# Performance work log

Measured on AMD Instinct MI355X. Metric: run time of the kernel, lower is better.

The kernel has to match this reference:

```python
import jax, jax.numpy as jnp
import numpy as np

N, E, DIN, DH, DOUT = 100000, 1600000, 512, 128, 40


def setup_inputs() -> dict:
    key = jax.random.key(0)
    ks = jax.random.split(key, 4)
    x = jax.random.normal(ks[0], (N, DIN), dtype=jnp.float32)
    edge_index = jax.random.randint(ks[1], (2, E), 0, N, dtype=jnp.int32)
    W1 = jax.random.normal(ks[2], (DIN, DH), dtype=jnp.float32) / np.sqrt(DIN).astype(np.float32)
    b1 = jnp.zeros((DH,), jnp.float32)
    W2 = jax.random.normal(ks[3], (DH, DOUT), dtype=jnp.float32) / np.sqrt(DH).astype(np.float32)
    b2 = jnp.zeros((DOUT,), jnp.float32)
    return {"x": x, "edge_index": edge_index, "W1": W1, "b1": b1, "W2": W2, "b2": b2}


def _gcn_conv(x, W, b, src, dst, norm, n):
    # PyG GCNConv: linear transform first, then normalized neighbor aggregation
    h = x @ W                                   # [n, d_out]
    msg = h[src] * norm[:, None]                # gather + scale, [E+n, d_out]
    out = jax.ops.segment_sum(msg, dst, num_segments=n)  # scatter-add
    return out + b


def reference(x, edge_index, W1, b1, W2, b2):
    n = x.shape[0]
    loops = jnp.arange(n, dtype=edge_index.dtype)
    src = jnp.concatenate([edge_index[0], loops])   # with self-loops
    dst = jnp.concatenate([edge_index[1], loops])
    deg = jax.ops.segment_sum(jnp.ones_like(dst, dtype=jnp.float32), dst, num_segments=n)
    dinv = jnp.where(deg > 0, jax.lax.rsqrt(jnp.maximum(deg, 1.0)), 0.0)
    norm = dinv[src] * dinv[dst]                    # deg^{-1/2}[j] * deg^{-1/2}[i]
    h = jax.nn.relu(_gcn_conv(x, W1, b1, src, dst, norm, n))
    # dropout p=0.5 is a no-op in eval mode (training=False)
    h = _gcn_conv(h, W2, b2, src, dst, norm, n)
    return h, jax.nn.log_softmax(h, axis=1)
```

## Files before the change

### kernel.cpp

```cpp
#include <hip/hip_runtime.h>
#include <math.h>


typedef unsigned int uint;
typedef unsigned short ushort_t;
using short8  = __attribute__((ext_vector_type(8))) short;
using float4v = __attribute__((ext_vector_type(4))) float;

__device__ __forceinline__ ushort_t f2bf(float f) {
    uint u = __float_as_uint(f);
    u += 0x7FFFu + ((u >> 16) & 1u);
    return (ushort_t)(u >> 16);
}
__device__ __forceinline__ float2 unpack2(uint v) {
    return make_float2(__uint_as_float(v << 16), __uint_as_float(v & 0xFFFF0000u));
}
__device__ __forceinline__ uint pack2(float a, float b) {
    return (uint)f2bf(a) | ((uint)f2bf(b) << 16);
}


__global__ __launch_bounds__(256) void k_bhist(const int* __restrict__ dst,
                                               int* __restrict__ bcnt, int e, int nb) {
    __shared__ int h[800];
    for (int t = threadIdx.x; t < nb; t += 256) h[t] = 0;
    __syncthreads();
    int ibase = blockIdx.x * 2560 + threadIdx.x;
#pragma unroll
    for (int j = 0; j < 10; j++) {
        int i = ibase + j * 256;
        if (i < e) atomicAdd(&h[dst[i] >> 7], 1);
    }
    __syncthreads();
    for (int t = threadIdx.x; t < nb; t += 256) {
        int c = h[t];
        if (c) atomicAdd(&bcnt[t], c);
    }
}

__global__ __launch_bounds__(256) void k_bscan(const int* __restrict__ bcnt, int* __restrict__ bbase,
                                               int* __restrict__ bcur, int* __restrict__ row_ptr,
                                               int nb, int n, int e) {
    __shared__ int sd[256];
    int t = threadIdx.x;
    int base = t * 4;
    int v[4];
#pragma unroll
    for (int j = 0; j < 4; j++) v[j] = (base + j < nb) ? bcnt[base + j] : 0;
    int s0 = v[0], s1 = s0 + v[1], s2 = s1 + v[2], s3 = s2 + v[3];
    sd[t] = s3;
    __syncthreads();
    for (int d = 1; d < 256; d <<= 1) {
        int x = (t >= d) ? sd[t - d] : 0;
        __syncthreads();
        sd[t] += x;
        __syncthreads();
    }
    int excl = sd[t] - s3;
    int pre0 = excl, pre1 = excl + s0, pre2 = excl + s1, pre3 = excl + s2;
    if (base + 0 < nb) { bbase[base + 0] = pre0; bcur[base + 0] = pre0; }
    if (base + 1 < nb) { bbase[base + 1] = pre1; bcur[base + 1] = pre1; }
    if (base + 2 < nb) { bbase[base + 2] = pre2; bcur[base + 2] = pre2; }
    if (base + 3 < nb) { bbase[base + 3] = pre3; bcur[base + 3] = pre3; }
    if (t == 255) bbase[nb] = excl + s3;
    if (t == 0) row_ptr[n] = e;
}

__global__ __launch_bounds__(256) void k_part(const int* __restrict__ src, const int* __restrict__ dst,
                                              int* __restrict__ bcur, uint* __restrict__ pbuf,
                                              int e, int nb) {
    __shared__ int h[800];
    __shared__ int base_l[800];
    for (int t = threadIdx.x; t < nb; t += 256) h[t] = 0;
    __syncthreads();
    uint pk[10]; int bk[10]; int lp[10];
    int ibase = blockIdx.x * 2560 + threadIdx.x;
#pragma unroll
    for (int j = 0; j < 10; j++) {
        int i = ibase + j * 256;
        bk[j] = -1;
        if (i < e) {
            int s = src[i], d = dst[i];
            int b = d >> 7;
            bk[j] = b;
            pk[j] = ((uint)(d & 127) << 25) | (uint)s;
            lp[j] = atomicAdd(&h[b], 1);
        }
    }
    __syncthreads();
    for (int t = threadIdx.x; t < nb; t += 256) {
        int c = h[t];
        base_l[t] = c ? atomicAdd(&bcur[t], c) : 0;
    }
    __syncthreads();
#pragma unroll
    for (int j = 0; j < 10; j++) {
        if (bk[j] >= 0) pbuf[base_l[bk[j]] + lp[j]] = pk[j];
    }
}

__global__ __launch_bounds__(256) void k_bsort(const uint* __restrict__ pbuf,
                                               const int* __restrict__ bbase,
                                               float* __restrict__ dinv,
                                               int* __restrict__ row_ptr,
                                               int* __restrict__ es_src, int n) {
    __shared__ int cl[128];
    __shared__ int cur[128];
    const int b = blockIdx.x;
    const int tid = threadIdx.x;
    const int ebeg = bbase[b], eend = bbase[b + 1];
    const int m = eend - ebeg;
    if (tid < 128) cl[tid] = 0;
    __syncthreads();
    for (int i = tid; i < m; i += 256) {
        uint p = pbuf[ebeg + i];
        atomicAdd(&cl[p >> 25], 1);
    }
    __syncthreads();
    int own = (tid < 128) ? cl[tid] : 0;
    for (int d = 1; d < 128; d <<= 1) {
        int v = 0;
        if (tid < 128 && tid >= d) v = cl[tid - d];
        __syncthreads();
        if (tid < 128 && tid >= d) cl[tid] += v;
        __syncthreads();
    }
    if (tid < 128) {
        int excl = cl[tid] - own;
        int node = b * 128 + tid;
        if (node < n) {
            dinv[node] = rsqrtf((float)(own + 1));
            row_ptr[node] = ebeg + excl;
        }
        cur[tid] = excl;
    }
    __syncthreads();
    for (int i = tid; i < m; i += 256) {
        uint p = pbuf[ebeg + i];
        int dl = (int)(p >> 25);
        int pos = atomicAdd(&cur[dl], 1);
        es_src[ebeg + pos] = (int)(p & 0x1FFFFFFu);
    }
}

__global__ __launch_bounds__(256) void k_wprep(const float* __restrict__ W1,
                                               const float* __restrict__ W2,
                                               ushort_t* __restrict__ W1t,
                                               ushort_t* __restrict__ W2t) {
    int idx = blockIdx.x * 256 + threadIdx.x;
    if (idx < 65536) {
        int nn = idx >> 9, k = idx & 511;
        W1t[idx] = f2bf(W1[(size_t)k * 128 + nn]);
    } else {
        int j = idx - 65536;
        if (j < 6144) {
            int c = j >> 7, k = j & 127;
            W2t[j] = (c < 40) ? f2bf(W2[(size_t)k * 40 + c]) : (ushort_t)0;
        }
    }
}

__global__ __launch_bounds__(256) void k_gemm1(const float* __restrict__ x,
                                               const ushort_t* __restrict__ W1t,
                                               const float* __restrict__ dinv,
                                               ushort_t* __restrict__ h, int n) {
    __shared__ ushort_t As[64][72];
    __shared__ ushort_t Bs[128][72];
    const int tid  = threadIdx.x;
    const int w    = tid >> 6, lane = tid & 63;
    const int quad = lane >> 4, l16 = lane & 15;
    const int row0 = blockIdx.x * 64;

    float4v acc[8];
#pragma unroll
    for (int i = 0; i < 8; i++) acc[i] = (float4v)0.f;

    const int ar  = tid >> 2;
    const int akq = (tid & 3) * 16;
    const int br  = tid >> 1;
    const int bkq = (tid & 1) * 32;
    const int agrow = row0 + ar;
    const float* xp0 = &x[(size_t)agrow * 512];
    const ushort_t* wp0 = &W1t[(size_t)br * 512];

    for (int kb = 0; kb < 512; kb += 64) {
#pragma unroll
        for (int j = 0; j < 4; j++) {
            float4 v = make_float4(0.f, 0.f, 0.f, 0.f);
            if (agrow < n) v = *(const float4*)(xp0 + kb + akq + j * 4);
            ushort4 b;
            b.x = f2bf(v.x); b.y = f2bf(v.y); b.z = f2bf(v.z); b.w = f2bf(v.w);
            *(ushort4*)&As[ar][akq + j * 4] = b;
        }
#pragma unroll
        for (int j = 0; j < 8; j++) {
            *(ushort4*)&Bs[br][bkq + j * 4] = *(const ushort4*)(wp0 + kb + bkq + j * 4);
        }
        __syncthreads();
#pragma unroll
        for (int ks = 0; ks < 64; ks += 32) {
            short8 a = *(const short8*)&As[w * 16 + l16][ks + quad * 8];
#pragma unroll
            for (int ct = 0; ct < 8; ct++) {
                short8 b = *(const short8*)&Bs[ct * 16 + l16][ks + quad * 8];
                acc[ct] = __builtin_amdgcn_mfma_f32_16x16x32_bf16(a, b, acc[ct], 0, 0, 0);
            }
        }
        __syncthreads();
    }
#pragma unroll
    for (int r = 0; r < 4; r++) {
        int grow = row0 + w * 16 + quad * 4 + r;
        if (grow >= n) continue;
        float di = dinv[grow];
#pragma unroll
        for (int ct = 0; ct < 8; ct++) {
            int col = ct * 16 + l16;
            h[(size_t)grow * 128 + col] = f2bf(di * acc[ct][r]);
        }
    }
}

__global__ __launch_bounds__(256) void k_agg1(const uint* __restrict__ h,
                                              const int* __restrict__ row_ptr,
                                              const int* __restrict__ es_src,
                                              const float* __restrict__ dinv,
                                              const float* __restrict__ b1,
                                              uint* __restrict__ h1, int n) {
    const int tid  = threadIdx.x;
    const int node = blockIdx.x * 4 + (tid >> 6);
    if (node >= n) return;
    const int lane = tid & 63;
    float2 acc = unpack2(h[(size_t)node * 64 + lane]);
    const int k0 = row_ptr[node], k1 = row_ptr[node + 1];
    int k = k0;
    for (; k + 3 < k1; k += 4) {
        int s0 = es_src[k], s1 = es_src[k + 1], s2 = es_src[k + 2], s3 = es_src[k + 3];
        float2 v0 = unpack2(h[(size_t)s0 * 64 + lane]);
        float2 v1 = unpack2(h[(size_t)s1 * 64 + lane]);
        float2 v2 = unpack2(h[(size_t)s2 * 64 + lane]);
        float2 v3 = unpack2(h[(size_t)s3 * 64 + lane]);
        acc.x += (v0.x + v1.x) + (v2.x + v3.x);
        acc.y += (v0.y + v1.y) + (v2.y + v3.y);
    }
    for (; k < k1; k++) {
        int s = es_src[k];
        float2 v = unpack2(h[(size_t)s * 64 + lane]);
        acc.x += v.x;
        acc.y += v.y;
    }
    const float di = dinv[node];
    float2 bb = *(const float2*)&b1[lane * 2];
    acc.x = di * acc.x + bb.x;
    acc.y = di * acc.y + bb.y;
    acc.x = acc.x > 0.f ? acc.x : 0.f;
    acc.y = acc.y > 0.f ? acc.y : 0.f;
    h1[(size_t)node * 64 + lane] = pack2(acc.x, acc.y);
}

__global__ __launch_bounds__(256) void k_gemm2(const ushort_t* __restrict__ h1,
                                               const ushort_t* __restrict__ W2t,
                                               const float* __restrict__ dinv,
                                               ushort_t* __restrict__ g, int n) {
    __shared__ ushort_t As[64][136];
    __shared__ ushort_t Bs[48][136];
    const int tid  = threadIdx.x;
    const int w    = tid >> 6, lane = tid & 63;
    const int quad = lane >> 4, l16 = lane & 15;
    const int row0 = blockIdx.x * 64;

    {
        int ar = tid >> 2;
        int ak = (tid & 3) * 32;
        int grow = row0 + ar;
#pragma unroll
        for (int j = 0; j < 4; j++) {
            uint4 v = make_uint4(0, 0, 0, 0);
            if (grow < n) v = *(const uint4*)&h1[(size_t)grow * 128 + ak + j * 8];
            *(uint4*)&As[ar][ak + j * 8] = v;
        }
    }
    for (int i = tid; i < 768; i += 256) {
        int row = i >> 4, q = i & 15;
        *(uint4*)&Bs[row][q * 8] = *(const uint4*)&W2t[(size_t)row * 128 + q * 8];
    }
    __syncthreads();

    float4v acc[3];
#pragma unroll
    for (int i = 0; i < 3; i++) acc[i] = (float4v)0.f;
#pragma unroll
    for (int ks = 0; ks < 128; ks += 32) {
        short8 a = *(const short8*)&As[w * 16 + l16][ks + quad * 8];
#pragma unroll
        for (int ct = 0; ct < 3; ct++) {
            short8 b = *(const short8*)&Bs[ct * 16 + l16][ks + quad * 8];
            acc[ct] = __builtin_amdgcn_mfma_f32_16x16x32_bf16(a, b, acc[ct], 0, 0, 0);
        }
    }
#pragma unroll
    for (int r = 0; r < 4; r++) {
        int grow = row0 + w * 16 + quad * 4 + r;
        if (grow >= n) continue;
        float di = dinv[grow];
#pragma unroll
        for (int ct = 0; ct < 3; ct++) {
            int col = ct * 16 + l16;
            g[(size_t)grow * 64 + col] = f2bf(di * acc[ct][r]);
        }
        g[(size_t)grow * 64 + 48 + l16] = (ushort_t)0;
    }
}

__global__ __launch_bounds__(256) void k_agg2(const uint* __restrict__ g,
                                              const int* __restrict__ row_ptr,
                                              const int* __restrict__ es_src,
                                              const float* __restrict__ dinv,
                                              const float* __restrict__ b2,
                                              float* __restrict__ out1,
                                              float* __restrict__ out2, int n) {
    const int tid  = threadIdx.x;
    const int node = blockIdx.x * 4 + (tid >> 6);
    if (node >= n) return;
    const int lane = tid & 63;
    const int half = lane >> 5;
    const int l    = lane & 31;

    float2 acc = make_float2(0.f, 0.f);
    if (half == 0) acc = unpack2(g[(size_t)node * 32 + l]);
    const int k0 = row_ptr[node], k1 = row_ptr[node + 1];
    int k = k0 + half;
    for (; k + 2 < k1; k += 4) {
        int s0 = es_src[k], s1 = es_src[k + 2];
        float2 v0 = unpack2(g[(size_t)s0 * 32 + l]);
        float2 v1 = unpack2(g[(size_t)s1 * 32 + l]);
        acc.x += v0.x + v1.x;
        acc.y += v0.y + v1.y;
    }
    for (; k < k1; k += 2) {
        float2 v = unpack2(g[(size_t)es_src[k] * 32 + l]);
        acc.x += v.x;
        acc.y += v.y;
    }
    acc.x += __shfl_xor(acc.x, 32);
    acc.y += __shfl_xor(acc.y, 32);

    const float di = dinv[node];
    float2 bb = (l < 20) ? *(const float2*)&b2[l * 2] : make_float2(0.f, 0.f);
    float v0 = di * acc.x + bb.x;
    float v1 = di * acc.y + bb.y;

    float m = (l < 20) ? fmaxf(v0, v1) : -1e30f;
#pragma unroll
    for (int d = 16; d; d >>= 1) m = fmaxf(m, __shfl_xor(m, d));
    float s = (l < 20) ? (expf(v0 - m) + expf(v1 - m)) : 0.f;
#pragma unroll
    for (int d = 16; d; d >>= 1) s += __shfl_xor(s, d);
    float ls = logf(s) + m;

    if (half == 0 && l < 20) {
        *(float2*)&out1[(size_t)node * 40 + l * 2] = make_float2(v0, v1);
        *(float2*)&out2[(size_t)node * 40 + l * 2] = make_float2(v0 - ls, v1 - ls);
    }
}

static inline size_t align4(size_t v) { return (v + 3) & ~(size_t)3; }

extern "C" void kernel_launch(void* const* d_in, const int* in_sizes, int n_in,
                              void* d_out, int out_size, void* d_ws, size_t ws_size,
                              hipStream_t stream) {
    const float* x  = (const float*)d_in[0];
    const int*   ei = (const int*)d_in[1];
    const float* W1 = (const float*)d_in[2];
    const float* b1 = (const float*)d_in[3];
    const float* W2 = (const float*)d_in[4];
    const float* b2 = (const float*)d_in[5];

    const int n = in_sizes[0] / 512;
    const int e = in_sizes[1] / 2;
    const int* src = ei;
    const int* dst = ei + e;
    const int NB = (n + 127) >> 7;

    char* p = (char*)d_ws;
    int*      bcnt    = (int*)p;        p += align4(NB) * 4;
    int*      bbase   = (int*)p;        p += align4(NB + 1) * 4;
    int*      bcur    = (int*)p;        p += align4(NB) * 4;
    int*      row_ptr = (int*)p;        p += align4(n + 1) * 4;
    float*    dinv    = (float*)p;      p += align4(n) * 4;
    uint*     pbuf    = (uint*)p;       p += align4(e) * 4;
    int*      es_src  = (int*)p;        p += align4(e) * 4;
    ushort_t* W1t     = (ushort_t*)p;   p += (size_t)128 * 512 * 2;
    ushort_t* W2t     = (ushort_t*)p;   p += (size_t)48 * 128 * 2;
    ushort_t* h       = (ushort_t*)p;   p += (size_t)n * 128 * 2;
    ushort_t* h1      = (ushort_t*)p;   p += (size_t)n * 128 * 2;
    ushort_t* g       = h;
    float*    out1    = (float*)d_out;
    float*    out2    = out1 + (size_t)n * 40;

    const int B = 256;
    const int nblkA = (e + 2559) / 2560;

    hipMemsetAsync(bcnt, 0, (size_t)NB * 4, stream);
    k_bhist<<<nblkA, B, 0, stream>>>(dst, bcnt, e, NB);
    k_bscan<<<1, 256, 0, stream>>>(bcnt, bbase, bcur, row_ptr, NB, n, e);
    k_part<<<nblkA, B, 0, stream>>>(src, dst, bcur, pbuf, e, NB);
    k_bsort<<<NB, 256, 0, stream>>>(pbuf, bbase, dinv, row_ptr, es_src, n);

    k_wprep<<<280, 256, 0, stream>>>(W1, W2, W1t, W2t);

    k_gemm1<<<(n + 63) / 64, 256, 0, stream>>>(x, W1t, dinv, h, n);
    k_agg1<<<(n + 3) / 4, 256, 0, stream>>>((const uint*)h, row_ptr, es_src, dinv, b1, (uint*)h1, n);

    k_gemm2<<<(n + 63) / 64, 256, 0, stream>>>(h1, W2t, dinv, g, n);
    k_agg2<<<(n + 3) / 4, 256, 0, stream>>>((const uint*)g, row_ptr, es_src, dinv, b2, out1, out2, n);
}
```

Before: 560.6 us.

## Vectorize gather in aggregation kernels and fold weight prep into histogram

```diff
diff --git a/kernel.cpp b/kernel.cpp
--- a/kernel.cpp
+++ b/kernel.cpp
@@ -18,10 +18,34 @@
 __device__ __forceinline__ uint pack2(float a, float b) {
     return (uint)f2bf(a) | ((uint)f2bf(b) << 16);
 }
-
-
-__global__ __launch_bounds__(256) void k_bhist(const int* __restrict__ dst,
-                                               int* __restrict__ bcnt, int e, int nb) {
+__device__ __forceinline__ void acc8(float* acc, uint4 v) {
+    float2 a0 = unpack2(v.x), a1 = unpack2(v.y), a2 = unpack2(v.z), a3 = unpack2(v.w);
+    acc[0] += a0.x; acc[1] += a0.y; acc[2] += a1.x; acc[3] += a1.y;
+    acc[4] += a2.x; acc[5] += a2.y; acc[6] += a3.x; acc[7] += a3.y;
+}
+
+
+__global__ __launch_bounds__(256) void k_bhist_wprep(const int* __restrict__ dst,
+                                                     int* __restrict__ bcnt, int e, int nb,
+                                                     int nblkA,
+                                                     const float* __restrict__ W1,
+                                                     const float* __restrict__ W2,
+                                                     ushort_t* __restrict__ W1t,
+                                                     ushort_t* __restrict__ W2t) {
+    if (blockIdx.x >= (uint)nblkA) {
+        int idx = (blockIdx.x - nblkA) * 256 + threadIdx.x;
+        if (idx < 65536) {
+            int nn = idx >> 9, k = idx & 511;
+            W1t[idx] = f2bf(W1[(size_t)k * 128 + nn]);
+        } else {
+            int j = idx - 65536;
+            if (j < 6144) {
+                int c = j >> 7, k = j & 127;
+                W2t[j] = (c < 40) ? f2bf(W2[(size_t)k * 40 + c]) : (ushort_t)0;
+            }
+        }
+        return;
+    }
     __shared__ int h[800];
     for (int t = threadIdx.x; t < nb; t += 256) h[t] = 0;
     __syncthreads();
@@ -143,23 +167,6 @@
     }
 }
 
-__global__ __launch_bounds__(256) void k_wprep(const float* __restrict__ W1,
-                                               const float* __restrict__ W2,
-                                               ushort_t* __restrict__ W1t,
-                                               ushort_t* __restrict__ W2t) {
-    int idx = blockIdx.x * 256 + threadIdx.x;
-    if (idx < 65536) {
-        int nn = idx >> 9, k = idx & 511;
-        W1t[idx] = f2bf(W1[(size_t)k * 128 + nn]);
-    } else {
-        int j = idx - 65536;
-        if (j < 6144) {
-            int c = j >> 7, k = j & 127;
-            W2t[j] = (c < 40) ? f2bf(W2[(size_t)k * 40 + c]) : (ushort_t)0;
-        }
-    }
-}
-
 __global__ __launch_bounds__(256) void k_gemm1(const float* __restrict__ x,
                                                const ushort_t* __restrict__ W1t,
                                                const float* __restrict__ dinv,
@@ -231,31 +238,55 @@
     const int node = blockIdx.x * 4 + (tid >> 6);
     if (node >= n) return;
     const int lane = tid & 63;
-    float2 acc = unpack2(h[(size_t)node * 64 + lane]);
+    const int g4   = lane >> 4;
+    const int l16  = lane & 15;
     const int k0 = row_ptr[node], k1 = row_ptr[node + 1];
-    int k = k0;
-    for (; k + 3 < k1; k += 4) {
-        int s0 = es_src[k], s1 = es_src[k + 1], s2 = es_src[k + 2], s3 = es_src[k + 3];
-        float2 v0 = unpack2(h[(size_t)s0 * 64 + lane]);
-        float2 v1 = unpack2(h[(size_t)s1 * 64 + lane]);
-        float2 v2 = unpack2(h[(size_t)s2 * 64 + lane]);
-        float2 v3 = unpack2(h[(size_t)s3 * 64 + lane]);
-        acc.x += (v0.x + v1.x) + (v2.x + v3.x);
-        acc.y += (v0.y + v1.y) + (v2.y + v3.y);
-    }
-    for (; k < k1; k++) {
-        int s = es_src[k];
-        float2 v = unpack2(h[(size_t)s * 64 + lane]);
-        acc.x += v.x;
-        acc.y += v.y;
-    }
+
+    uint4 sv = *(const uint4*)&h[(size_t)node * 64 + l16 * 4];
+
+    float acc[8];
+#pragma unroll
+    for (int i = 0; i < 8; i++) acc[i] = 0.f;
+
+    int k = k0 + g4;
+    for (; k + 4 < k1; k += 8) {
+        int s0 = es_src[k];
+        int s1 = es_src[k + 4];
+        uint4 v0 = *(const uint4*)&h[(size_t)s0 * 64 + l16 * 4];
+        uint4 v1 = *(const uint4*)&h[(size_t)s1 * 64 + l16 * 4];
+        acc8(acc, v0);
+        acc8(acc, v1);
+    }
+    for (; k < k1; k += 4) {
+        int s0 = es_src[k];
+        uint4 v0 = *(const uint4*)&h[(size_t)s0 * 64 + l16 * 4];
+        acc8(acc, v0);
+    }
+
+#pragma unroll
+    for (int i = 0; i < 8; i++) {
+        acc[i] += __shfl_xor(acc[i], 16);
+        acc[i] += __shfl_xor(acc[i], 32);
+    }
+    acc8(acc, sv);
+
     const float di = dinv[node];
-    float2 bb = *(const float2*)&b1[lane * 2];
-    acc.x = di * acc.x + bb.x;
-    acc.y = di * acc.y + bb.y;
-    acc.x = acc.x > 0.f ? acc.x : 0.f;
-    acc.y = acc.y > 0.f ? acc.y : 0.f;
-    h1[(size_t)node * 64 + lane] = pack2(acc.x, acc.y);
+    float4 ba = *(const float4*)&b1[l16 * 8];
+    float4 bb = *(const float4*)&b1[l16 * 8 + 4];
+    float r[8];
+    r[0] = di * acc[0] + ba.x; r[1] = di * acc[1] + ba.y;
+    r[2] = di * acc[2] + ba.z; r[3] = di * acc[3] + ba.w;
+    r[4] = di * acc[4] + bb.x; r[5] = di * acc[5] + bb.y;
+    r[6] = di * acc[6] + bb.z; r[7] = di * acc[7] + bb.w;
+#pragma unroll
+    for (int i = 0; i < 8; i++) r[i] = r[i] > 0.f ? r[i] : 0.f;
+
+    if (g4 == 0) {
+        uint4 o;
+        o.x = pack2(r[0], r[1]); o.y = pack2(r[2], r[3]);
+        o.z = pack2(r[4], r[5]); o.w = pack2(r[6], r[7]);
+        *(uint4*)&h1[(size_t)node * 64 + l16 * 4] = o;
+    }
 }
 
 __global__ __launch_bounds__(256) void k_gemm2(const ushort_t* __restrict__ h1,
@@ -323,44 +354,79 @@
     const int node = blockIdx.x * 4 + (tid >> 6);
     if (node >= n) return;
     const int lane = tid & 63;
-    const int half = lane >> 5;
-    const int l    = lane & 31;
-
-    float2 acc = make_float2(0.f, 0.f);
-    if (half == 0) acc = unpack2(g[(size_t)node * 32 + l]);
+    const int g8   = lane >> 3;
+    const int l8   = lane & 7;
     const int k0 = row_ptr[node], k1 = row_ptr[node + 1];
-    int k = k0 + half;
-    for (; k + 2 < k1; k += 4) {
-        int s0 = es_src[k], s1 = es_src[k + 2];
-        float2 v0 = unpack2(g[(size_t)s0 * 32 + l]);
-        float2 v1 = unpack2(g[(size_t)s1 * 32 + l]);
-        acc.x += v0.x + v1.x;
-        acc.y += v0.y + v1.y;
-    }
-    for (; k < k1; k += 2) {
-        float2 v = unpack2(g[(size_t)es_src[k] * 32 + l]);
-        acc.x += v.x;
-        acc.y += v.y;
-    }
-    acc.x += __shfl_xor(acc.x, 32);
-    acc.y += __shfl_xor(acc.y, 32);
+
+    uint4 sv = *(const uint4*)&g[(size_t)node * 32 + l8 * 4];
+
+    float acc[8];
+#pragma unroll
+    for (int i = 0; i < 8; i++) acc[i] = 0.f;
+
+    int k = k0 + g8;
+    for (; k + 8 < k1; k += 16) {
+        int s0 = es_src[k];
+        int s1 = es_src[k + 8];
+        uint4 v0 = *(const uint4*)&g[(size_t)s0 * 32 + l8 * 4];
+        uint4 v1 = *(const uint4*)&g[(size_t)s1 * 32 + l8 * 4];
+        acc8(acc, v0);
+        acc8(acc, v1);
+    }
+    for (; k < k1; k += 8) {
+        int s0 = es_src[k];
+        uint4 v0 = *(const uint4*)&g[(size_t)s0 * 32 + l8 * 4];
+        acc8(acc, v0);
+    }
+
+#pragma unroll
+    for (int i = 0; i < 8; i++) {
+        acc[i] += __shfl_xor(acc[i], 8);
+        acc[i] += __shfl_xor(acc[i], 16);
+        acc[i] += __shfl_xor(acc[i], 32);
+    }
+    acc8(acc, sv);
 
     const float di = dinv[node];
-    float2 bb = (l < 20) ? *(const float2*)&b2[l * 2] : make_float2(0.f, 0.f);
-    float v0 = di * acc.x + bb.x;
-    float v1 = di * acc.y + bb.y;
-
-    float m = (l < 20) ? fmaxf(v0, v1) : -1e30f;
-#pragma unroll
-    for (int d = 16; d; d >>= 1) m = fmaxf(m, __shfl_xor(m, d));
-    float s = (l < 20) ? (expf(v0 - m) + expf(v1 - m)) : 0.f;
-#pragma unroll
-    for (int d = 16; d; d >>= 1) s += __shfl_xor(s, d);
+    float v[8];
+    if (l8 < 5) {
+        float4 ba = *(const float4*)&b2[l8 * 8];
+        float4 bb = *(const float4*)&b2[l8 * 8 + 4];
+        v[0] = di * acc[0] + ba.x; v[1] = di * acc[1] + ba.y;
+        v[2] = di * acc[2] + ba.z; v[3] = di * acc[3] + ba.w;
+        v[4] = di * acc[4] + bb.x; v[5] = di * acc[5] + bb.y;
+        v[6] = di * acc[6] + bb.z; v[7] = di * acc[7] + bb.w;
+    } else {
+#pragma unroll
+        for (int i = 0; i < 8; i++) v[i] = 0.f;
+    }
+
+    float m = -1e30f;
+    if (l8 < 5) {
+#pragma unroll
+        for (int i = 0; i < 8; i++) m = fmaxf(m, v[i]);
+    }
+#pragma unroll
+    for (int d = 1; d < 8; d <<= 1) m = fmaxf(m, __shfl_xor(m, d));
+    float s = 0.f;
+    if (l8 < 5) {
+#pragma unroll
+        for (int i = 0; i < 8; i++) s += expf(v[i] - m);
+    }
+#pragma unroll
+    for (int d = 1; d < 8; d <<= 1) s += __shfl_xor(s, d);
     float ls = logf(s) + m;
 
-    if (half == 0 && l < 20) {
-        *(float2*)&out1[(size_t)node * 40 + l * 2] = make_float2(v0, v1);
-        *(float2*)&out2[(size_t)node * 40 + l * 2] = make_float2(v0 - ls, v1 - ls);
+    if (l8 < 5) {
+        if (g8 == 0) {
+            *(float4*)&out1[(size_t)node * 40 + l8 * 8]     = make_float4(v[0], v[1], v[2], v[3]);
+            *(float4*)&out1[(size_t)node * 40 + l8 * 8 + 4] = make_float4(v[4], v[5], v[6], v[7]);
+        } else if (g8 == 1) {
+            *(float4*)&out2[(size_t)node * 40 + l8 * 8] =
+                make_float4(v[0] - ls, v[1] - ls, v[2] - ls, v[3] - ls);
+            *(float4*)&out2[(size_t)node * 40 + l8 * 8 + 4] =
+                make_float4(v[4] - ls, v[5] - ls, v[6] - ls, v[7] - ls);
+        }
     }
 }
 
@@ -402,13 +468,11 @@
     const int nblkA = (e + 2559) / 2560;
 
     hipMemsetAsync(bcnt, 0, (size_t)NB * 4, stream);
-    k_bhist<<<nblkA, B, 0, stream>>>(dst, bcnt, e, NB);
+    k_bhist_wprep<<<nblkA + 280, B, 0, stream>>>(dst, bcnt, e, NB, nblkA, W1, W2, W1t, W2t);
     k_bscan<<<1, 256, 0, stream>>>(bcnt, bbase, bcur, row_ptr, NB, n, e);
     k_part<<<nblkA, B, 0, stream>>>(src, dst, bcur, pbuf, e, NB);
     k_bsort<<<NB, 256, 0, stream>>>(pbuf, bbase, dinv, row_ptr, es_src, n);
 
-    k_wprep<<<280, 256, 0, stream>>>(W1, W2, W1t, W2t);
-
     k_gemm1<<<(n + 63) / 64, 256, 0, stream>>>(x, W1t, dinv, h, n);
     k_agg1<<<(n + 3) / 4, 256, 0, stream>>>((const uint*)h, row_ptr, es_src, dinv, b1, (uint*)h1, n);
 
```

Result: faster. 535.1 us (-4.6%).
